# Performance work log

Hardware: AMD Instinct MI355X
Metric: run time of the kernel (lower is better)

## Reference

```python
import jax, jax.numpy as jnp
import numpy as np
import math

DIM = 1024
HEADS = 16
DHEAD = 64
WINDOW = 512
STRIDE = 32


def setup_inputs() -> dict:
    key = jax.random.key(0)
    ks = jax.random.split(key, 4)
    x = jax.random.normal(ks[0], (2, 4096, DIM), dtype=jnp.float32)
    W_qkv = jax.random.normal(ks[1], (DIM, 3 * HEADS * DHEAD), dtype=jnp.float32) * 0.02
    W_gate = jax.random.normal(ks[2], (DIM, 1), dtype=jnp.float32) * 0.02
    b_gate = jnp.zeros((1,), dtype=jnp.float32)
    W_out = jax.random.normal(ks[3], (HEADS * DHEAD, DIM), dtype=jnp.float32) * 0.02
    b_out = jnp.zeros((DIM,), dtype=jnp.float32)
    return {"x": x, "W_qkv": W_qkv, "W_gate": W_gate, "b_gate": b_gate,
            "W_out": W_out, "b_out": b_out}


def _local_attention(q, k, v):
    # q,k,v: [b, s, h, d]; overlapping windows: query block W attends K/V block [i-W/2, i+W+W/2)
    b, s, h, d = q.shape
    W = WINDOW
    half = W // 2
    nW = s // W
    scale = 1.0 / math.sqrt(d)
    k_pad = jnp.pad(k, ((0, 0), (half, half), (0, 0), (0, 0)))
    v_pad = jnp.pad(v, ((0, 0), (half, half), (0, 0), (0, 0)))
    # gather each window's 2W-wide K/V block
    idx = jnp.arange(nW)[:, None] * W + jnp.arange(2 * W)[None, :]  # [nW, 2W]
    kb = k_pad[:, idx]  # [b, nW, 2W, h, d]
    vb = v_pad[:, idx]
    qb = q.reshape(b, nW, W, h, d)
    scores = jnp.einsum('bnwhd,bnthd->bnwht', qb, kb) * scale  # [b,nW,W,h,2W]
    valid = (idx >= half) & (idx < s + half)  # mask out zero padding at edges
    scores = jnp.where(valid[None, :, None, None, :], scores, jnp.float32(-1e9))
    attn = jax.nn.softmax(scores, axis=-1)
    out = jnp.einsum('bnwht,bnthd->bnwhd', attn, vb)
    return out.reshape(b, s, h, d)


def _sparse_global_attention(q, k, v):
    b, s, h, d = q.shape
    scale = 1.0 / math.sqrt(d)
    k_str = k[:, ::STRIDE]  # [b, s/STRIDE, h, d]
    v_str = v[:, ::STRIDE]
    scores = jnp.einsum('bshd,bthd->bsht', q, k_str) * scale
    attn = jax.nn.softmax(scores, axis=-1)
    return jnp.einsum('bsht,bthd->bshd', attn, v_str)


def reference(x, W_qkv, W_gate, b_gate, W_out, b_out):
    b, s, dim = x.shape
    qkv = x @ W_qkv  # [b, s, 3*h*d]
    q, k, v = jnp.split(qkv, 3, axis=-1)
    q = q.reshape(b, s, HEADS, DHEAD)
    k = k.reshape(b, s, HEADS, DHEAD)
    v = v.reshape(b, s, HEADS, DHEAD)
    local_out = _local_attention(q, k, v)
    global_out = _sparse_global_attention(q, k, v)
    combine = jax.nn.sigmoid(x @ W_gate + b_gate)  # [b, s, 1]
    gate = combine[..., None]  # [b, s, 1, 1] broadcasts over heads, dim_head
    out = gate * local_out + (1.0 - gate) * global_out
    out = out.reshape(b, s, HEADS * DHEAD)
    return out @ W_out + b_out
```

## Files before the change

kernel.cpp:

```cpp
#include <hip/hip_runtime.h>
#include <hip/hip_bf16.h>
#include <cstdint>
#include <cstddef>

typedef __attribute__((ext_vector_type(8))) short bfrag;
typedef __attribute__((ext_vector_type(4))) short short4v;
typedef __attribute__((ext_vector_type(4))) float facc;

static __device__ __forceinline__ short f2bf(float f) {
  __hip_bfloat16 h = __float2bfloat16(f);
  return *reinterpret_cast<short*>(&h);
}
static __device__ __forceinline__ float bf2f(short s) {
  union { float f; unsigned int u; } c; c.u = ((unsigned int)(unsigned short)s) << 16;
  return c.f;
}

static __device__ __forceinline__ void gload16(const short* g, short* l) {
  __builtin_amdgcn_global_load_lds(
      (const __attribute__((address_space(1))) unsigned int*)(g),
      (__attribute__((address_space(3))) unsigned int*)(l), 16, 0, 0);
}

#define SL 0.18033688011112043f

__global__ __launch_bounds__(256) void cvt_rows_gate(
    const float* __restrict__ src, short* __restrict__ dst,
    const float* __restrict__ Wg, const float* __restrict__ bg,
    float* __restrict__ g) {
  const int t = threadIdx.x;
  size_t i = (size_t)blockIdx.x * 256 + t;
  const facc* s4 = (const facc*)src;
  facc v0 = s4[i * 2], v1 = s4[i * 2 + 1];
  bfrag o;
  o[0] = f2bf(v0[0]); o[1] = f2bf(v0[1]); o[2] = f2bf(v0[2]); o[3] = f2bf(v0[3]);
  o[4] = f2bf(v1[0]); o[5] = f2bf(v1[1]); o[6] = f2bf(v1[2]); o[7] = f2bf(v1[3]);
  *(bfrag*)(dst + i * 8) = o;
  const facc* wr = (const facc*)(Wg + (t & 127) * 8);
  facc w0 = wr[0], w1 = wr[1];
  float s = v0[0]*w0[0] + v0[1]*w0[1] + v0[2]*w0[2] + v0[3]*w0[3]
          + v1[0]*w1[0] + v1[1]*w1[1] + v1[2]*w1[2] + v1[3]*w1[3];
  #pragma unroll
  for (int mm = 1; mm < 64; mm <<= 1) s += __shfl_xor(s, mm);
  __shared__ float gsum[4];
  if ((t & 63) == 0) gsum[t >> 6] = s;
  __syncthreads();
  if ((t & 127) == 0) {
    int half = t >> 7;
    float tot = gsum[half * 2] + gsum[half * 2 + 1] + bg[0];
    g[blockIdx.x * 2 + half] = 1.f / (1.f + __expf(-tot));
  }
}

__global__ __launch_bounds__(256) void cvt_T(const float* __restrict__ src,
                                             short* __restrict__ dst, int N, int K) {
  __shared__ short tile[64][65];
  int n0 = blockIdx.x * 64, k0 = blockIdx.y * 64;
  int tx = threadIdx.x & 63, ty = threadIdx.x >> 6;
  #pragma unroll
  for (int i = ty; i < 64; i += 4)
    tile[i][tx] = f2bf(src[(size_t)(k0 + i) * N + n0 + tx]);
  __syncthreads();
  #pragma unroll
  for (int i = ty; i < 64; i += 4)
    dst[(size_t)(n0 + i) * K + k0 + tx] = tile[tx][i];
}

__global__ __launch_bounds__(256) void prep_attn(
    const short* __restrict__ kb, const short* __restrict__ vb,
    short* __restrict__ vbt, short* __restrict__ vgt, short* __restrict__ kgs) {
  __shared__ short tile[64][65];
  const int t = threadIdx.x, tx = t & 63, ty = t >> 6;
  const int k0 = blockIdx.x * 64, bh = blockIdx.y;
  const size_t base = (size_t)bh * 262144;
  #pragma unroll
  for (int i = ty; i < 64; i += 4)
    tile[i][tx] = vb[base + (size_t)(k0 + i) * 64 + tx];
  __syncthreads();
  #pragma unroll
  for (int i = ty; i < 64; i += 4)
    vbt[base + (size_t)i * 4096 + k0 + tx] = tile[tx][i];
  if (t < 128) {
    int sk = t >> 6, d = t & 63;
    int gi = (k0 >> 5) + sk;
    vgt[(size_t)bh * 8192 + d * 128 + gi] = tile[sk * 32][d];
    kgs[(size_t)bh * 8192 + gi * 64 + d] = kb[base + (size_t)(k0 + sk * 32) * 64 + d];
  }
}

template <int EPI>
__global__ __launch_bounds__(256) void gemm_bt(
    const short* __restrict__ A, const short* __restrict__ Bt,
    int M, int N, int K,
    short* __restrict__ q_out, short* __restrict__ k_out, short* __restrict__ v_out,
    float* __restrict__ out, const float* __restrict__ bias) {
  __shared__ short Ab[2][128 * 32];
  __shared__ short Bb[2][128 * 32];
  const int t = threadIdx.x;
  const int l = t & 63;
  const int tile_m = blockIdx.y * 128;
  const int tile_n = blockIdx.x * 128;
  const int w = t >> 6;
  const int wm = (w >> 1) * 64, wn = (w & 1) * 64;
  const int c0 = t, c1 = t + 256;

  facc acc[4][4];
  #pragma unroll
  for (int i = 0; i < 4; ++i)
    #pragma unroll
    for (int j = 0; j < 4; ++j) acc[i][j] = (facc){0.f, 0.f, 0.f, 0.f};

  const short* Abase = A + (size_t)tile_m * K;
  const short* Bbase = Bt + (size_t)tile_n * K;
  const size_t ga0 = (size_t)(c0 >> 2) * K + (c0 & 3) * 8;
  const size_t ga1 = (size_t)(c1 >> 2) * K + (c1 & 3) * 8;

  auto stage = [&](int k0, int buf) {
    gload16(Abase + ga0 + k0, &Ab[buf][c0 * 8]);
    gload16(Abase + ga1 + k0, &Ab[buf][c1 * 8]);
    gload16(Bbase + ga0 + k0, &Bb[buf][c0 * 8]);
    gload16(Bbase + ga1 + k0, &Bb[buf][c1 * 8]);
  };

  stage(0, 0);
  __syncthreads();
  int buf = 0;
  for (int k0 = 0; k0 < K; k0 += 32) {
    if (k0 + 32 < K) stage(k0 + 32, buf ^ 1);
    bfrag af[4], bf[4];
    #pragma unroll
    for (int i = 0; i < 4; ++i)
      af[i] = *(const bfrag*)&Ab[buf][(wm + i * 16 + (l & 15)) * 32 + ((l >> 4) << 3)];
    #pragma unroll
    for (int i = 0; i < 4; ++i)
      bf[i] = *(const bfrag*)&Bb[buf][(wn + i * 16 + (l & 15)) * 32 + ((l >> 4) << 3)];
    #pragma unroll
    for (int mt = 0; mt < 4; ++mt)
      #pragma unroll
      for (int nt = 0; nt < 4; ++nt)
        acc[mt][nt] = __builtin_amdgcn_mfma_f32_16x16x32_bf16(af[mt], bf[nt], acc[mt][nt], 0, 0, 0);
    __syncthreads();
    buf ^= 1;
  }

  #pragma unroll
  for (int mt = 0; mt < 4; ++mt)
    #pragma unroll
    for (int nt = 0; nt < 4; ++nt) {
      int col = tile_n + wn + nt * 16 + (l & 15);
      int row0 = tile_m + wm + mt * 16 + ((l >> 4) << 2);
      if (EPI == 0) {
        int which = col >> 10, rem = col & 1023, hh = rem >> 6, dd = rem & 63;
        short* dst = (which == 0) ? q_out : ((which == 1) ? k_out : v_out);
        float vsc = (which == 0) ? SL : 1.f;
        #pragma unroll
        for (int r = 0; r < 4; ++r) {
          int m = row0 + r, b = m >> 12, s = m & 4095;
          dst[(((size_t)b * 16 + hh) * 4096 + s) * 64 + dd] = f2bf(acc[mt][nt][r] * vsc);
        }
      } else {
        float bv = bias[col];
        #pragma unroll
        for (int r = 0; r < 4; ++r)
          out[(size_t)(row0 + r) * N + col] = acc[mt][nt][r] + bv;
      }
    }
}


__global__ __launch_bounds__(256) void attn_fused(
    const short* __restrict__ qg, const short* __restrict__ kg,
    const short* __restrict__ vbt, const short* __restrict__ vgt,
    const short* __restrict__ kgs,
    const float* __restrict__ gate, short* __restrict__ comb) {
  __shared__ short Kt[2][64 * 64];
  __shared__ short Vt[2][64 * 64];
  __shared__ short Pb[4][16 * 64];

  const int t = threadIdx.x, l = t & 63, w = t >> 6;
  const int bid = blockIdx.x;
  const int yy = bid >> 3;
  const int bh = (bid & 7) * 4 + (yy >> 5);
  const int qblk = yy & 31;
  const int q0 = qblk * 128;
  const int b = bh >> 4, h = bh & 15;
  const int lo = l & 15, hi = l >> 4, hi4 = (l >> 4) << 2;

  const int n = q0 >> 9;
  int kstart = n * 512 - 256; if (kstart < 0) kstart = 0;
  int kend = n * 512 + 768; if (kend > 4096) kend = 4096;
  const int nloc = (kend - kstart) >> 6;

  const size_t qrow = (size_t)bh * 4096 + q0 + w * 32;
  bfrag qf[2][2];
  #pragma unroll
  for (int mt = 0; mt < 2; ++mt)
    #pragma unroll
    for (int hf = 0; hf < 2; ++hf)
      qf[mt][hf] = *(const bfrag*)(qg + (qrow + mt * 16 + lo) * 64 + hf * 32 + hi * 8);

  bfrag ones;
  #pragma unroll
  for (int i = 0; i < 8; ++i) ones[i] = (short)0x3F80;

  facc ls_l[2], ls_g[2];
  facc o_l[2][4], o_g[2][4];
  #pragma unroll
  for (int mt = 0; mt < 2; ++mt) {
    ls_l[mt] = (facc){0.f, 0.f, 0.f, 0.f};
    ls_g[mt] = (facc){0.f, 0.f, 0.f, 0.f};
    #pragma unroll
    for (int nt = 0; nt < 4; ++nt) {
      o_l[mt][nt] = (facc){0.f, 0.f, 0.f, 0.f};
      o_g[mt][nt] = (facc){0.f, 0.f, 0.f, 0.f};
    }
  }

  const int c0 = t, c1 = t + 256;
  const int r0 = c0 >> 3, r1 = c1 >> 3;
  const int s0 = (c0 & 7) ^ ((r0 & 7) ^ (r0 >> 3));
  const int s1 = (c1 & 7) ^ ((r1 & 7) ^ (r1 >> 3));

  const size_t kBaseL = (size_t)bh * 262144;
  const size_t sBase  = (size_t)bh * 8192;

  auto stageLoc = [&](int itl, int buf) {
    const int col = kstart + itl * 64;
    gload16(kg  + kBaseL + (size_t)(col + r0) * 64 + s0 * 8, &Kt[buf][c0 * 8]);
    gload16(kg  + kBaseL + (size_t)(col + r1) * 64 + s1 * 8, &Kt[buf][c1 * 8]);
    gload16(vbt + kBaseL + (size_t)r0 * 4096 + col + s0 * 8, &Vt[buf][c0 * 8]);
    gload16(vbt + kBaseL + (size_t)r1 * 4096 + col + s1 * 8, &Vt[buf][c1 * 8]);
  };
  auto stageGlb = [&](int itg, int buf) {
    gload16(kgs + sBase + (size_t)(itg * 64 + r0) * 64 + s0 * 8, &Kt[buf][c0 * 8]);
    gload16(kgs + sBase + (size_t)(itg * 64 + r1) * 64 + s1 * 8, &Kt[buf][c1 * 8]);
    gload16(vgt + sBase + (size_t)r0 * 128 + itg * 64 + s0 * 8, &Vt[buf][c0 * 8]);
    gload16(vgt + sBase + (size_t)r1 * 128 + itg * 64 + s1 * 8, &Vt[buf][c1 * 8]);
  };

  const int gq = (lo & 7) ^ (lo >> 3);
  auto computeTile = [&](int buf, facc (&ls)[2], facc (&oacc)[2][4]) {
    bfrag kf[4][2];
    #pragma unroll
    for (int kt = 0; kt < 4; ++kt) {
      int key = kt * 16 + lo; int gk2 = (key & 7) ^ (key >> 3);
      const short* Kr = &Kt[buf][key * 64];
      kf[kt][0] = *(const bfrag*)&Kr[(hi * 8) ^ (gk2 << 3)];
      kf[kt][1] = *(const bfrag*)&Kr[(32 + hi * 8) ^ (gk2 << 3)];
    }
    bfrag vf[4][2];
    #pragma unroll
    for (int nt = 0; nt < 4; ++nt) {
      int d = nt * 16 + lo; int gd = (d & 7) ^ (d >> 3);
      const short* Vr = &Vt[buf][d * 64];
      vf[nt][0] = *(const bfrag*)&Vr[(hi * 8) ^ (gd << 3)];
      vf[nt][1] = *(const bfrag*)&Vr[(32 + hi * 8) ^ (gd << 3)];
    }
    short* Pw = &Pb[w][0];
    #pragma unroll
    for (int mt = 0; mt < 2; ++mt) {
      facc sA[4];
      #pragma unroll
      for (int kt = 0; kt < 4; ++kt) {
        facc z = (facc){0.f, 0.f, 0.f, 0.f};
        z = __builtin_amdgcn_mfma_f32_16x16x32_bf16(kf[kt][0], qf[mt][0], z, 0, 0, 0);
        z = __builtin_amdgcn_mfma_f32_16x16x32_bf16(kf[kt][1], qf[mt][1], z, 0, 0, 0);
        sA[kt] = z;
      }
      short4v pk[4];
      #pragma unroll
      for (int kt = 0; kt < 4; ++kt)
        #pragma unroll
        for (int r = 0; r < 4; ++r)
          pk[kt][r] = f2bf(exp2f(sA[kt][r]));
      #pragma unroll
      for (int kt = 0; kt < 4; ++kt)
        *(short4v*)&Pw[lo * 64 + ((kt * 16 + hi4) ^ (gq << 3))] = pk[kt];
      bfrag pf0 = *(const bfrag*)&Pw[lo * 64 + ((hi * 8) ^ (gq << 3))];
      bfrag pf1 = *(const bfrag*)&Pw[lo * 64 + ((32 + hi * 8) ^ (gq << 3))];
      ls[mt] = __builtin_amdgcn_mfma_f32_16x16x32_bf16(pf0, ones, ls[mt], 0, 0, 0);
      ls[mt] = __builtin_amdgcn_mfma_f32_16x16x32_bf16(pf1, ones, ls[mt], 0, 0, 0);
      #pragma unroll
      for (int nt = 0; nt < 4; ++nt) {
        facc oo = oacc[mt][nt];
        oo = __builtin_amdgcn_mfma_f32_16x16x32_bf16(pf0, vf[nt][0], oo, 0, 0, 0);
        oo = __builtin_amdgcn_mfma_f32_16x16x32_bf16(pf1, vf[nt][1], oo, 0, 0, 0);
        oacc[mt][nt] = oo;
      }
    }
  };

  stageGlb(0, 0);
  __syncthreads();
  stageGlb(1, 1);
  computeTile(0, ls_g, o_g);
  __syncthreads();
  stageLoc(0, 0);
  computeTile(1, ls_g, o_g);

  unsigned ogp[2][8];
  #pragma unroll
  for (int mt = 0; mt < 2; ++mt) {
    float inv[4];
    #pragma unroll
    for (int r = 0; r < 4; ++r) inv[r] = 1.f / ls_g[mt][r];
    #pragma unroll
    for (int nt = 0; nt < 4; ++nt)
      #pragma unroll
      for (int rp = 0; rp < 2; ++rp) {
        unsigned a = (unsigned short)f2bf(o_g[mt][nt][rp * 2] * inv[rp * 2]);
        unsigned bq = (unsigned short)f2bf(o_g[mt][nt][rp * 2 + 1] * inv[rp * 2 + 1]);
        ogp[mt][nt * 2 + rp] = a | (bq << 16);
      }
  }
  __syncthreads();

  int buf = 0;
  for (int itl = 0; itl < nloc; ++itl) {
    if (itl + 1 < nloc) stageLoc(itl + 1, buf ^ 1);
    computeTile(buf, ls_l, o_l);
    __syncthreads();
    buf ^= 1;
  }

  #pragma unroll
  for (int mt = 0; mt < 2; ++mt) {
    #pragma unroll
    for (int r = 0; r < 4; ++r) {
      float invl = 1.f / ls_l[mt][r];
      int q = q0 + w * 32 + mt * 16 + hi4 + r;
      float gg = gate[b * 4096 + q];
      size_t obase = ((size_t)b * 4096 + q) * 1024 + h * 64;
      #pragma unroll
      for (int nt = 0; nt < 4; ++nt) {
        unsigned pw = ogp[mt][nt * 2 + (r >> 1)];
        float og = bf2f((short)((r & 1) ? (pw >> 16) : (pw & 0xffff)));
        float val = gg * o_l[mt][nt][r] * invl + (1.f - gg) * og;
        comb[obase + nt * 16 + lo] = f2bf(val);
      }
    }
  }
}

extern "C" void kernel_launch(void* const* d_in, const int* in_sizes, int n_in,
                              void* d_out, int out_size, void* d_ws, size_t ws_size,
                              hipStream_t stream) {
  const float* x    = (const float*)d_in[0];
  const float* Wqkv = (const float*)d_in[1];
  const float* Wg   = (const float*)d_in[2];
  const float* bg   = (const float*)d_in[3];
  const float* Wout = (const float*)d_in[4];
  const float* bout = (const float*)d_in[5];
  float* out = (float*)d_out;

  char* p = (char*)d_ws;
  short* xbf   = (short*)p; p += (size_t)8192 * 1024 * 2;
  short* WqkvT = (short*)p; p += (size_t)3072 * 1024 * 2;
  short* WoutT = (short*)p; p += (size_t)1024 * 1024 * 2;
  short* qb    = (short*)p; p += (size_t)32 * 4096 * 64 * 2;
  short* kb    = (short*)p; p += (size_t)32 * 4096 * 64 * 2;
  short* vb    = (short*)p; p += (size_t)32 * 4096 * 64 * 2;
  float* g     = (float*)p; p += (size_t)8192 * 4;
  short* vbt   = (short*)p; p += (size_t)32 * 64 * 4096 * 2;
  short* comb  = xbf;
  short* vgt   = WqkvT;
  short* kgs   = WqkvT + (size_t)32 * 64 * 128;

  cvt_rows_gate<<<4096, 256, 0, stream>>>(x, xbf, Wg, bg, g);
  cvt_T<<<dim3(48, 16), 256, 0, stream>>>(Wqkv, WqkvT, 3072, 1024);
  cvt_T<<<dim3(16, 16), 256, 0, stream>>>(Wout, WoutT, 1024, 1024);
  gemm_bt<0><<<dim3(24, 64), 256, 0, stream>>>(xbf, WqkvT, 8192, 3072, 1024,
                                               qb, kb, vb, nullptr, nullptr);
  prep_attn<<<dim3(64, 32), 256, 0, stream>>>(kb, vb, vbt, vgt, kgs);
  attn_fused<<<1024, 256, 0, stream>>>(qb, kb, vbt, vgt, kgs, g, comb);
  gemm_bt<1><<<dim3(8, 64), 256, 0, stream>>>(comb, WoutT, 8192, 1024, 1024,
                                              nullptr, nullptr, nullptr, out, bout);
}
```

Measured before the change: 282.1 us.

## Use 8 waves per attention block with one 16-row tile each; merge transposes

The attention kernel now launches 512 threads (8 waves), and each wave handles one 16-query MFMA tile instead of two. This halves per-wave accumulator registers, and each thread issues one staging load per K/V tile instead of two. The aim is more waves in flight to hide latency, at the cost of each wave reusing its LDS K/V fragment reads over fewer query rows and barriers spanning more waves. The two weight-transpose launches are also merged into one kernel to save a launch.

```diff
diff --git a/kernel.cpp b/kernel.cpp
--- a/kernel.cpp
+++ b/kernel.cpp
@@ -52,10 +52,15 @@
   }
 }
 
-__global__ __launch_bounds__(256) void cvt_T(const float* __restrict__ src,
-                                             short* __restrict__ dst, int N, int K) {
+__global__ __launch_bounds__(256) void cvt_T2(
+    const float* __restrict__ s1, short* __restrict__ d1,
+    const float* __restrict__ s2, short* __restrict__ d2) {
   __shared__ short tile[64][65];
-  int n0 = blockIdx.x * 64, k0 = blockIdx.y * 64;
+  const int bx = blockIdx.x;
+  const float* src; short* dst; int N; int n0;
+  if (bx < 48) { src = s1; dst = d1; N = 3072; n0 = bx * 64; }
+  else         { src = s2; dst = d2; N = 1024; n0 = (bx - 48) * 64; }
+  int k0 = blockIdx.y * 64;
   int tx = threadIdx.x & 63, ty = threadIdx.x >> 6;
   #pragma unroll
   for (int i = ty; i < 64; i += 4)
@@ -63,7 +68,7 @@
   __syncthreads();
   #pragma unroll
   for (int i = ty; i < 64; i += 4)
-    dst[(size_t)(n0 + i) * K + k0 + tx] = tile[tx][i];
+    dst[(size_t)(n0 + i) * 1024 + k0 + tx] = tile[tx][i];
 }
 
 __global__ __launch_bounds__(256) void prep_attn(
@@ -168,14 +173,14 @@
 }
 
 
-__global__ __launch_bounds__(256) void attn_fused(
+__global__ __launch_bounds__(512) void attn_fused(
     const short* __restrict__ qg, const short* __restrict__ kg,
     const short* __restrict__ vbt, const short* __restrict__ vgt,
     const short* __restrict__ kgs,
     const float* __restrict__ gate, short* __restrict__ comb) {
   __shared__ short Kt[2][64 * 64];
   __shared__ short Vt[2][64 * 64];
-  __shared__ short Pb[4][16 * 64];
+  __shared__ short Pb[8][16 * 64];
 
   const int t = threadIdx.x, l = t & 63, w = t >> 6;
   const int bid = blockIdx.x;
@@ -191,55 +196,43 @@
   int kend = n * 512 + 768; if (kend > 4096) kend = 4096;
   const int nloc = (kend - kstart) >> 6;
 
-  const size_t qrow = (size_t)bh * 4096 + q0 + w * 32;
-  bfrag qf[2][2];
-  #pragma unroll
-  for (int mt = 0; mt < 2; ++mt)
-    #pragma unroll
-    for (int hf = 0; hf < 2; ++hf)
-      qf[mt][hf] = *(const bfrag*)(qg + (qrow + mt * 16 + lo) * 64 + hf * 32 + hi * 8);
+  const size_t qrow = (size_t)bh * 4096 + q0 + w * 16;
+  bfrag qf[2];
+  #pragma unroll
+  for (int hf = 0; hf < 2; ++hf)
+    qf[hf] = *(const bfrag*)(qg + (qrow + lo) * 64 + hf * 32 + hi * 8);
 
   bfrag ones;
   #pragma unroll
   for (int i = 0; i < 8; ++i) ones[i] = (short)0x3F80;
 
-  facc ls_l[2], ls_g[2];
-  facc o_l[2][4], o_g[2][4];
-  #pragma unroll
-  for (int mt = 0; mt < 2; ++mt) {
-    ls_l[mt] = (facc){0.f, 0.f, 0.f, 0.f};
-    ls_g[mt] = (facc){0.f, 0.f, 0.f, 0.f};
-    #pragma unroll
-    for (int nt = 0; nt < 4; ++nt) {
-      o_l[mt][nt] = (facc){0.f, 0.f, 0.f, 0.f};
-      o_g[mt][nt] = (facc){0.f, 0.f, 0.f, 0.f};
-    }
-  }
-
-  const int c0 = t, c1 = t + 256;
-  const int r0 = c0 >> 3, r1 = c1 >> 3;
-  const int s0 = (c0 & 7) ^ ((r0 & 7) ^ (r0 >> 3));
-  const int s1 = (c1 & 7) ^ ((r1 & 7) ^ (r1 >> 3));
+  facc ls_l = (facc){0.f, 0.f, 0.f, 0.f};
+  facc ls_g = (facc){0.f, 0.f, 0.f, 0.f};
+  facc o_l[4], o_g[4];
+  #pragma unroll
+  for (int nt = 0; nt < 4; ++nt) {
+    o_l[nt] = (facc){0.f, 0.f, 0.f, 0.f};
+    o_g[nt] = (facc){0.f, 0.f, 0.f, 0.f};
+  }
+
+  const int c = t, r = c >> 3;
+  const int sl = (c & 7) ^ ((r & 7) ^ (r >> 3));
 
   const size_t kBaseL = (size_t)bh * 262144;
   const size_t sBase  = (size_t)bh * 8192;
 
   auto stageLoc = [&](int itl, int buf) {
     const int col = kstart + itl * 64;
-    gload16(kg  + kBaseL + (size_t)(col + r0) * 64 + s0 * 8, &Kt[buf][c0 * 8]);
-    gload16(kg  + kBaseL + (size_t)(col + r1) * 64 + s1 * 8, &Kt[buf][c1 * 8]);
-    gload16(vbt + kBaseL + (size_t)r0 * 4096 + col + s0 * 8, &Vt[buf][c0 * 8]);
-    gload16(vbt + kBaseL + (size_t)r1 * 4096 + col + s1 * 8, &Vt[buf][c1 * 8]);
+    gload16(kg  + kBaseL + (size_t)(col + r) * 64 + sl * 8, &Kt[buf][c * 8]);
+    gload16(vbt + kBaseL + (size_t)r * 4096 + col + sl * 8, &Vt[buf][c * 8]);
   };
   auto stageGlb = [&](int itg, int buf) {
-    gload16(kgs + sBase + (size_t)(itg * 64 + r0) * 64 + s0 * 8, &Kt[buf][c0 * 8]);
-    gload16(kgs + sBase + (size_t)(itg * 64 + r1) * 64 + s1 * 8, &Kt[buf][c1 * 8]);
-    gload16(vgt + sBase + (size_t)r0 * 128 + itg * 64 + s0 * 8, &Vt[buf][c0 * 8]);
-    gload16(vgt + sBase + (size_t)r1 * 128 + itg * 64 + s1 * 8, &Vt[buf][c1 * 8]);
+    gload16(kgs + sBase + (size_t)(itg * 64 + r) * 64 + sl * 8, &Kt[buf][c * 8]);
+    gload16(vgt + sBase + (size_t)r * 128 + itg * 64 + sl * 8, &Vt[buf][c * 8]);
   };
 
   const int gq = (lo & 7) ^ (lo >> 3);
-  auto computeTile = [&](int buf, facc (&ls)[2], facc (&oacc)[2][4]) {
+  auto computeTile = [&](int buf, facc& ls, facc (&oacc)[4]) {
     bfrag kf[4][2];
     #pragma unroll
     for (int kt = 0; kt < 4; ++kt) {
@@ -257,36 +250,33 @@
       vf[nt][1] = *(const bfrag*)&Vr[(32 + hi * 8) ^ (gd << 3)];
     }
     short* Pw = &Pb[w][0];
-    #pragma unroll
-    for (int mt = 0; mt < 2; ++mt) {
-      facc sA[4];
+    facc sA[4];
+    #pragma unroll
+    for (int kt = 0; kt < 4; ++kt) {
+      facc z = (facc){0.f, 0.f, 0.f, 0.f};
+      z = __builtin_amdgcn_mfma_f32_16x16x32_bf16(kf[kt][0], qf[0], z, 0, 0, 0);
+      z = __builtin_amdgcn_mfma_f32_16x16x32_bf16(kf[kt][1], qf[1], z, 0, 0, 0);
+      sA[kt] = z;
+    }
+    short4v pk[4];
+    #pragma unroll
+    for (int kt = 0; kt < 4; ++kt)
       #pragma unroll
-      for (int kt = 0; kt < 4; ++kt) {
-        facc z = (facc){0.f, 0.f, 0.f, 0.f};
-        z = __builtin_amdgcn_mfma_f32_16x16x32_bf16(kf[kt][0], qf[mt][0], z, 0, 0, 0);
-        z = __builtin_amdgcn_mfma_f32_16x16x32_bf16(kf[kt][1], qf[mt][1], z, 0, 0, 0);
-        sA[kt] = z;
-      }
-      short4v pk[4];
-      #pragma unroll
-      for (int kt = 0; kt < 4; ++kt)
-        #pragma unroll
-        for (int r = 0; r < 4; ++r)
-          pk[kt][r] = f2bf(exp2f(sA[kt][r]));
-      #pragma unroll
-      for (int kt = 0; kt < 4; ++kt)
-        *(short4v*)&Pw[lo * 64 + ((kt * 16 + hi4) ^ (gq << 3))] = pk[kt];
-      bfrag pf0 = *(const bfrag*)&Pw[lo * 64 + ((hi * 8) ^ (gq << 3))];
-      bfrag pf1 = *(const bfrag*)&Pw[lo * 64 + ((32 + hi * 8) ^ (gq << 3))];
-      ls[mt] = __builtin_amdgcn_mfma_f32_16x16x32_bf16(pf0, ones, ls[mt], 0, 0, 0);
-      ls[mt] = __builtin_amdgcn_mfma_f32_16x16x32_bf16(pf1, ones, ls[mt], 0, 0, 0);
-      #pragma unroll
-      for (int nt = 0; nt < 4; ++nt) {
-        facc oo = oacc[mt][nt];
-        oo = __builtin_amdgcn_mfma_f32_16x16x32_bf16(pf0, vf[nt][0], oo, 0, 0, 0);
-        oo = __builtin_amdgcn_mfma_f32_16x16x32_bf16(pf1, vf[nt][1], oo, 0, 0, 0);
-        oacc[mt][nt] = oo;
-      }
+      for (int rr = 0; rr < 4; ++rr)
+        pk[kt][rr] = f2bf(exp2f(sA[kt][rr]));
+    #pragma unroll
+    for (int kt = 0; kt < 4; ++kt)
+      *(short4v*)&Pw[lo * 64 + ((kt * 16 + hi4) ^ (gq << 3))] = pk[kt];
+    bfrag pf0 = *(const bfrag*)&Pw[lo * 64 + ((hi * 8) ^ (gq << 3))];
+    bfrag pf1 = *(const bfrag*)&Pw[lo * 64 + ((32 + hi * 8) ^ (gq << 3))];
+    ls = __builtin_amdgcn_mfma_f32_16x16x32_bf16(pf0, ones, ls, 0, 0, 0);
+    ls = __builtin_amdgcn_mfma_f32_16x16x32_bf16(pf1, ones, ls, 0, 0, 0);
+    #pragma unroll
+    for (int nt = 0; nt < 4; ++nt) {
+      facc oo = oacc[nt];
+      oo = __builtin_amdgcn_mfma_f32_16x16x32_bf16(pf0, vf[nt][0], oo, 0, 0, 0);
+      oo = __builtin_amdgcn_mfma_f32_16x16x32_bf16(pf1, vf[nt][1], oo, 0, 0, 0);
+      oacc[nt] = oo;
     }
   };
 
@@ -298,19 +288,18 @@
   stageLoc(0, 0);
   computeTile(1, ls_g, o_g);
 
-  unsigned ogp[2][8];
-  #pragma unroll
-  for (int mt = 0; mt < 2; ++mt) {
+  unsigned ogp[8];
+  {
     float inv[4];
     #pragma unroll
-    for (int r = 0; r < 4; ++r) inv[r] = 1.f / ls_g[mt][r];
+    for (int rr = 0; rr < 4; ++rr) inv[rr] = 1.f / ls_g[rr];
     #pragma unroll
     for (int nt = 0; nt < 4; ++nt)
       #pragma unroll
       for (int rp = 0; rp < 2; ++rp) {
-        unsigned a = (unsigned short)f2bf(o_g[mt][nt][rp * 2] * inv[rp * 2]);
-        unsigned bq = (unsigned short)f2bf(o_g[mt][nt][rp * 2 + 1] * inv[rp * 2 + 1]);
-        ogp[mt][nt * 2 + rp] = a | (bq << 16);
+        unsigned a = (unsigned short)f2bf(o_g[nt][rp * 2] * inv[rp * 2]);
+        unsigned bq = (unsigned short)f2bf(o_g[nt][rp * 2 + 1] * inv[rp * 2 + 1]);
+        ogp[nt * 2 + rp] = a | (bq << 16);
       }
   }
   __syncthreads();
@@ -324,20 +313,17 @@
   }
 
   #pragma unroll
-  for (int mt = 0; mt < 2; ++mt) {
-    #pragma unroll
-    for (int r = 0; r < 4; ++r) {
-      float invl = 1.f / ls_l[mt][r];
-      int q = q0 + w * 32 + mt * 16 + hi4 + r;
-      float gg = gate[b * 4096 + q];
-      size_t obase = ((size_t)b * 4096 + q) * 1024 + h * 64;
-      #pragma unroll
-      for (int nt = 0; nt < 4; ++nt) {
-        unsigned pw = ogp[mt][nt * 2 + (r >> 1)];
-        float og = bf2f((short)((r & 1) ? (pw >> 16) : (pw & 0xffff)));
-        float val = gg * o_l[mt][nt][r] * invl + (1.f - gg) * og;
-        comb[obase + nt * 16 + lo] = f2bf(val);
-      }
+  for (int rr = 0; rr < 4; ++rr) {
+    float invl = 1.f / ls_l[rr];
+    int q = q0 + w * 16 + hi4 + rr;
+    float gg = gate[b * 4096 + q];
+    size_t obase = ((size_t)b * 4096 + q) * 1024 + h * 64;
+    #pragma unroll
+    for (int nt = 0; nt < 4; ++nt) {
+      unsigned pw = ogp[nt * 2 + (rr >> 1)];
+      float og = bf2f((short)((rr & 1) ? (pw >> 16) : (pw & 0xffff)));
+      float val = gg * o_l[nt][rr] * invl + (1.f - gg) * og;
+      comb[obase + nt * 16 + lo] = f2bf(val);
     }
   }
 }
@@ -367,12 +353,11 @@
   short* kgs   = WqkvT + (size_t)32 * 64 * 128;
 
   cvt_rows_gate<<<4096, 256, 0, stream>>>(x, xbf, Wg, bg, g);
-  cvt_T<<<dim3(48, 16), 256, 0, stream>>>(Wqkv, WqkvT, 3072, 1024);
-  cvt_T<<<dim3(16, 16), 256, 0, stream>>>(Wout, WoutT, 1024, 1024);
+  cvt_T2<<<dim3(64, 16), 256, 0, stream>>>(Wqkv, WqkvT, Wout, WoutT);
   gemm_bt<0><<<dim3(24, 64), 256, 0, stream>>>(xbf, WqkvT, 8192, 3072, 1024,
                                                qb, kb, vb, nullptr, nullptr);
   prep_attn<<<dim3(64, 32), 256, 0, stream>>>(kb, vb, vbt, vgt, kgs);
-  attn_fused<<<1024, 256, 0, stream>>>(qb, kb, vbt, vgt, kgs, g, comb);
+  attn_fused<<<1024, 512, 0, stream>>>(qb, kb, vbt, vgt, kgs, g, comb);
   gemm_bt<1><<<dim3(8, 64), 256, 0, stream>>>(comb, WoutT, 8192, 1024, 1024,
                                               nullptr, nullptr, nullptr, out, bout);
 }
```

Measured after the change: 274.1 us. -2.8%, faster.
